# Kernel optimization log

Measured on AMD Instinct MI355X. Metric: run time of the kernel, lower is better.

The kernel has to match this reference:

```python
import jax, jax.numpy as jnp
import numpy as np

DIM_IN = 768
DIM_OUT = 64
SEQ = 4096
BATCH = 4

def setup_inputs() -> dict:
    key = jax.random.key(0)
    ks = jax.random.split(key, 7)
    s = 1.0 / np.sqrt(DIM_IN)
    return {
        "x": jax.random.normal(ks[0], (BATCH, SEQ, DIM_IN), dtype=jnp.float32),
        "wq": jax.random.uniform(ks[1], (DIM_IN, DIM_OUT), jnp.float32, -s, s),
        "bq": jax.random.uniform(ks[2], (DIM_OUT,), jnp.float32, -s, s),
        "wk": jax.random.uniform(ks[3], (DIM_IN, DIM_OUT), jnp.float32, -s, s),
        "bk": jax.random.uniform(ks[4], (DIM_OUT,), jnp.float32, -s, s),
        "wv": jax.random.uniform(ks[5], (DIM_IN, DIM_OUT), jnp.float32, -s, s),
        "bv": jax.random.uniform(ks[6], (DIM_OUT,), jnp.float32, -s, s),
    }

def reference(x, wq, bq, wk, bk, wv, bv):
    # QKV projections: (B, S, D_in) @ (D_in, D_out) + bias
    q = x @ wq + bq
    k = x @ wk + bk
    v = x @ wv + bv
    # full causal attention, scores scaled by sqrt(d_out) AFTER masking (as in source)
    scores = jnp.einsum('bqd,bkd->bqk', q, k)  # (B, S, S)
    seq = x.shape[1]
    causal = jnp.tril(jnp.ones((seq, seq), dtype=bool))  # True = keep
    scores = jnp.where(causal, scores, -jnp.inf)
    scale = 1.0 / np.sqrt(k.shape[-1]).astype(np.float32)
    weights = jax.nn.softmax(scores * scale, axis=-1)
    # dropout_rate = 0.0 -> identity
    return jnp.einsum('bqk,bkd->bqd', weights, v)
```

## Files before the change

### kernel.cpp

```cpp
#include <hip/hip_runtime.h>
#include <hip/hip_bf16.h>

#define BATCH 4
#define SEQ   4096
#define DIN   768
#define DOUT  64

typedef __attribute__((ext_vector_type(4))) float f32x4;
typedef __attribute__((ext_vector_type(8))) short short8;
typedef __attribute__((ext_vector_type(4))) short short4v;

#define QSCALE 0.18033688011112043f

static __device__ __forceinline__ unsigned short f2bf(float f) {
    union { float f; unsigned u; } un; un.f = f;
    unsigned r = un.u + 0x7FFF + ((un.u >> 16) & 1);
    return (unsigned short)(r >> 16);
}
static __device__ __forceinline__ float bf2f(unsigned short h) {
    union { unsigned u; float f; } un; un.u = ((unsigned)h) << 16;
    return un.f;
}

__global__ void wprep_kernel(const float* __restrict__ wq,
                             const float* __restrict__ wk,
                             const float* __restrict__ wv,
                             unsigned short* __restrict__ wF) {
    __shared__ float lds[64][65];
    int o = blockIdx.x / 12, kt = blockIdx.x % 12;
    const float* w = (o == 0) ? wq : (o == 1) ? wk : wv;
    int tid = threadIdx.x;
    int k0 = kt * 64;
    #pragma unroll
    for (int i = 0; i < 16; ++i) {
        int flat = tid + i * 256;
        int kl = flat >> 6, n = flat & 63;
        lds[kl][n] = w[(k0 + kl) * 64 + n];
    }
    __syncthreads();
    int lane = tid & 63;
    int m = lane & 15, g = lane >> 4;
    #pragma unroll
    for (int i = 0; i < 2; ++i) {
        int f = i * 4 + (tid >> 6);
        int t = f >> 1, kcl = f & 1;
        int kc = kt * 2 + kcl;
        int nc = o * 4 + t;
        short8 v;
        #pragma unroll
        for (int j = 0; j < 8; ++j)
            v[j] = (short)f2bf(lds[kcl * 32 + g * 8 + j][t * 16 + m]);
        *(short8*)&wF[(size_t)(nc * 24 + kc) * 512 + lane * 8] = v;
    }
}

__global__ void __launch_bounds__(256) proj_kernel(
        const float* __restrict__ x,
        const float* __restrict__ bq,
        const float* __restrict__ bk,
        const float* __restrict__ bv,
        const unsigned short* __restrict__ wF,
        unsigned short* __restrict__ Qf,
        unsigned short* __restrict__ Kf,
        unsigned short* __restrict__ Vf) {
    __shared__ __align__(16) unsigned short xs[16][776];
    __shared__ unsigned short tr[4][16][24];

    int tid = threadIdx.x;
    int w = tid >> 6;
    int lane = tid & 63;
    int m = lane & 15, g = lane >> 4;
    int r0 = blockIdx.x * 16;

    {
        const float* xbase = x + (size_t)r0 * DIN;
        #pragma unroll
        for (int i = 0; i < 12; ++i) {
            int flat4 = tid + i * 256;
            int row = flat4 / 192;
            int c4 = flat4 - row * 192;
            float4 v = *(const float4*)(xbase + (size_t)row * DIN + c4 * 4);
            short4v sv;
            sv[0] = (short)f2bf(v.x); sv[1] = (short)f2bf(v.y);
            sv[2] = (short)f2bf(v.z); sv[3] = (short)f2bf(v.w);
            *(short4v*)&xs[row][c4 * 4] = sv;
        }
    }
    __syncthreads();

    f32x4 acc[3];
    #pragma unroll
    for (int t = 0; t < 3; ++t) acc[t] = (f32x4){0.f, 0.f, 0.f, 0.f};

    for (int kc = 0; kc < 24; ++kc) {
        short8 af = *(const short8*)&xs[m][kc * 32 + g * 8];
        #pragma unroll
        for (int tt = 0; tt < 3; ++tt) {
            int nc = w * 3 + tt;
            short8 bfrg = *(const short8*)(wF + (size_t)(nc * 24 + kc) * 512 + lane * 8);
            acc[tt] = __builtin_amdgcn_mfma_f32_16x16x32_bf16(af, bfrg, acc[tt], 0, 0, 0);
        }
    }

    int b2 = r0 >> 12;
    int ss = r0 & 4095;
    int s = ss >> 5, half = (ss >> 4) & 1;
    #pragma unroll
    for (int tt = 0; tt < 3; ++tt) {
        int nc = w * 3 + tt;
        int o = nc >> 2;
        int t = nc & 3;
        const float* bias_p = (o == 0) ? bq : (o == 1) ? bk : bv;
        float bias = bias_p[t * 16 + m];
        #pragma unroll
        for (int r = 0; r < 4; ++r) {
            float val = acc[tt][r] + bias;
            if (o == 0) val *= QSCALE;
            tr[w][g * 4 + r][m] = f2bf(val);
        }
        if (o < 2) {
            if (g < 2) {
                short8 v8;
                #pragma unroll
                for (int j = 0; j < 8; ++j) v8[j] = (short)tr[w][m][g * 8 + j];
                unsigned short* dst = (o == 0) ? Qf : Kf;
                int c = t >> 1;
                *(short8*)&dst[(size_t)(blockIdx.x * 2 + c) * 512
                               + (((t & 1) * 2 + g) * 16 + m) * 8] = v8;
            }
        } else {
            if (g < 2) {
                short8 v8;
                #pragma unroll
                for (int j = 0; j < 8; ++j) v8[j] = (short)tr[w][g * 8 + j][m];
                *(short8*)&Vf[((size_t)(b2 * 128 + s) * 4 + t) * 512
                              + ((half * 2 + g) * 16 + m) * 8] = v8;
            }
        }
    }
}

__global__ void __launch_bounds__(512, 4) attn_kernel(
        const unsigned short* __restrict__ Qf,
        const unsigned short* __restrict__ Kf,
        const unsigned short* __restrict__ Vf,
        float* __restrict__ out) {
    __shared__ __align__(16) unsigned short P_lds[8][32][36];
    __shared__ __align__(16) unsigned short pacc[8][16][68];
    __shared__ float pm[8][16];
    __shared__ float pl[8][16];

    int j = blockIdx.x;
    int b = (j & 7) >> 1;
    int pair = 127 - ((j >> 3) * 2 + (j & 1));
    int q0 = pair * 32;
    int nsteps = pair + 1;
    int tid = threadIdx.x;
    int w = tid >> 6;
    int lane = tid & 63;
    int m = lane & 15, g = lane >> 4;

    const unsigned short* Qbase = Qf + (size_t)(b * 256 + pair * 2) * 1024 + lane * 8;
    short8 qf[2][2];
    qf[0][0] = *(const short8*)(Qbase);
    qf[0][1] = *(const short8*)(Qbase + 512);
    qf[1][0] = *(const short8*)(Qbase + 1024);
    qf[1][1] = *(const short8*)(Qbase + 1536);

    short8 onesB = (short8){0,0,0,0,0,0,0,0};
    if (m == 0) {
        #pragma unroll
        for (int jj = 0; jj < 8; ++jj) onesB[jj] = (short)0x3F80;
    }

    f32x4 acc[2][5];
    #pragma unroll
    for (int rt = 0; rt < 2; ++rt)
        #pragma unroll
        for (int t = 0; t < 5; ++t) acc[rt][t] = (f32x4){0.f, 0.f, 0.f, 0.f};
    float mrun[2][4];
    #pragma unroll
    for (int rt = 0; rt < 2; ++rt)
        #pragma unroll
        for (int r = 0; r < 4; ++r) mrun[rt][r] = -INFINITY;

    const unsigned short* Kbase = Kf + (size_t)(b * 256) * 1024 + lane * 8;
    const unsigned short* Vbase = Vf + (size_t)(b * 128) * 2048 + lane * 8;

    for (int s = w; s < nsteps; s += 8) {
        int kv0 = s * 32;
        short8 kf[4];
        kf[0] = *(const short8*)(Kbase + (size_t)s * 2048);
        kf[1] = *(const short8*)(Kbase + (size_t)s * 2048 + 512);
        kf[2] = *(const short8*)(Kbase + (size_t)s * 2048 + 1024);
        kf[3] = *(const short8*)(Kbase + (size_t)s * 2048 + 1536);
        short8 vcur[4];
        #pragma unroll
        for (int t = 0; t < 4; ++t)
            vcur[t] = *(const short8*)(Vbase + (size_t)s * 2048 + t * 512);
        bool last = (s == nsteps - 1);

        #pragma unroll
        for (int rt = 0; rt < 2; ++rt) {
            f32x4 sc[2];
            sc[0] = (f32x4){0.f, 0.f, 0.f, 0.f};
            sc[1] = (f32x4){0.f, 0.f, 0.f, 0.f};
            sc[0] = __builtin_amdgcn_mfma_f32_16x16x32_bf16(qf[rt][0], kf[0], sc[0], 0, 0, 0);
            sc[0] = __builtin_amdgcn_mfma_f32_16x16x32_bf16(qf[rt][1], kf[1], sc[0], 0, 0, 0);
            sc[1] = __builtin_amdgcn_mfma_f32_16x16x32_bf16(qf[rt][0], kf[2], sc[1], 0, 0, 0);
            sc[1] = __builtin_amdgcn_mfma_f32_16x16x32_bf16(qf[rt][1], kf[3], sc[1], 0, 0, 0);

            if (last) {
                #pragma unroll
                for (int tt = 0; tt < 2; ++tt)
                    #pragma unroll
                    for (int r = 0; r < 4; ++r)
                        if (kv0 + tt * 16 + m > q0 + rt * 16 + g * 4 + r) sc[tt][r] = -INFINITY;
            }

            bool need = false;
            #pragma unroll
            for (int r = 0; r < 4; ++r) {
                float th = mrun[rt][r] + 8.0f;
                need = need | (sc[0][r] > th) | (sc[1][r] > th);
            }
            if (__any(need)) {
                float rmax[4];
                #pragma unroll
                for (int r = 0; r < 4; ++r) rmax[r] = fmaxf(sc[0][r], sc[1][r]);
                #pragma unroll
                for (int msk = 1; msk <= 8; msk <<= 1)
                    #pragma unroll
                    for (int r = 0; r < 4; ++r)
                        rmax[r] = fmaxf(rmax[r], __shfl_xor(rmax[r], msk));
                #pragma unroll
                for (int r = 0; r < 4; ++r) {
                    float mnew = fmaxf(mrun[rt][r], rmax[r]);
                    float alpha = __builtin_amdgcn_exp2f(mrun[rt][r] - mnew);
                    mrun[rt][r] = mnew;
                    #pragma unroll
                    for (int t = 0; t < 5; ++t) acc[rt][t][r] *= alpha;
                }
            }

            #pragma unroll
            for (int tt = 0; tt < 2; ++tt)
                #pragma unroll
                for (int r = 0; r < 4; ++r)
                    P_lds[w][rt * 16 + g * 4 + r][tt * 16 + m] =
                        f2bf(__builtin_amdgcn_exp2f(sc[tt][r] - mrun[rt][r]));
            short8 pa = *(const short8*)&P_lds[w][rt * 16 + m][g * 8];

            #pragma unroll
            for (int t = 0; t < 4; ++t)
                acc[rt][t] = __builtin_amdgcn_mfma_f32_16x16x32_bf16(pa, vcur[t], acc[rt][t], 0, 0, 0);
            acc[rt][4] = __builtin_amdgcn_mfma_f32_16x16x32_bf16(pa, onesB, acc[rt][4], 0, 0, 0);
        }
    }

    #pragma unroll
    for (int rt = 0; rt < 2; ++rt) {
        if (m == 0) {
            #pragma unroll
            for (int r = 0; r < 4; ++r) {
                pm[w][g * 4 + r] = mrun[rt][r];
                pl[w][g * 4 + r] = acc[rt][4][r];
            }
        }
        #pragma unroll
        for (int t = 0; t < 4; ++t)
            #pragma unroll
            for (int r = 0; r < 4; ++r)
                pacc[w][g * 4 + r][t * 16 + m] = f2bf(acc[rt][t][r]);
        __syncthreads();

        if (tid < 256) {
            int row = tid >> 4;
            int c4 = (tid & 15) * 4;
            float mmax = pm[0][row];
            #pragma unroll
            for (int w2 = 1; w2 < 8; ++w2) mmax = fmaxf(mmax, pm[w2][row]);
            float lt = 0.f;
            float o0 = 0.f, o1 = 0.f, o2 = 0.f, o3 = 0.f;
            #pragma unroll
            for (int w2 = 0; w2 < 8; ++w2) {
                float sc2 = __builtin_amdgcn_exp2f(pm[w2][row] - mmax);
                lt += pl[w2][row] * sc2;
                short4v pa4 = *(const short4v*)&pacc[w2][row][c4];
                o0 += bf2f((unsigned short)pa4[0]) * sc2;
                o1 += bf2f((unsigned short)pa4[1]) * sc2;
                o2 += bf2f((unsigned short)pa4[2]) * sc2;
                o3 += bf2f((unsigned short)pa4[3]) * sc2;
            }
            float invl = 1.0f / lt;
            float4 res = make_float4(o0 * invl, o1 * invl, o2 * invl, o3 * invl);
            *(float4*)&out[(size_t)(b * SEQ + q0 + rt * 16 + row) * DOUT + c4] = res;
        }
        __syncthreads();
    }
}

extern "C" void kernel_launch(void* const* d_in, const int* in_sizes, int n_in,
                              void* d_out, int out_size, void* d_ws, size_t ws_size,
                              hipStream_t stream) {
    const float* x  = (const float*)d_in[0];
    const float* wq = (const float*)d_in[1];
    const float* bq = (const float*)d_in[2];
    const float* wk = (const float*)d_in[3];
    const float* bk = (const float*)d_in[4];
    const float* wv = (const float*)d_in[5];
    const float* bv = (const float*)d_in[6];
    float* out = (float*)d_out;

    char* ws = (char*)d_ws;
    unsigned short* wF = (unsigned short*)ws;
    unsigned short* Qf = (unsigned short*)(ws + 294912);
    unsigned short* Kf = (unsigned short*)(ws + 294912 + 2097152);
    unsigned short* Vf = (unsigned short*)(ws + 294912 + 4194304);

    wprep_kernel<<<36, 256, 0, stream>>>(wq, wk, wv, wF);
    proj_kernel<<<1024, 256, 0, stream>>>(x, bq, bk, bv, wF, Qf, Kf, Vf);
    attn_kernel<<<512, 512, 0, stream>>>(Qf, Kf, Vf, out);
}
```

Measured before the change: 53.99 us.

## Prefetch next K/V tile in registers and interleave row-tile MFMAs

Software-pipelines the attention loop by loading the K and V fragments for the next step into registers while the current step computes, hiding global load latency. It also restructures the inner loop so both row tiles' QK MFMAs are issued first, then softmax for both, then the PV MFMAs interleaved across row tiles, which raises independent MFMA work available to the scheduler. The cost is higher register pressure from double-buffered K/V fragments and extra score registers, which could lower occupancy.

Result: slower. 109.6 us (+102.9%).

```diff
diff --git a/kernel.cpp b/kernel.cpp
--- a/kernel.cpp
+++ b/kernel.cpp
@@ -187,47 +187,61 @@
     const unsigned short* Kbase = Kf + (size_t)(b * 256) * 1024 + lane * 8;
     const unsigned short* Vbase = Vf + (size_t)(b * 128) * 2048 + lane * 8;
 
+    short8 kf[4], vf[4];
+    if (w < nsteps) {
+        #pragma unroll
+        for (int t = 0; t < 4; ++t) {
+            kf[t] = *(const short8*)(Kbase + (size_t)w * 2048 + t * 512);
+            vf[t] = *(const short8*)(Vbase + (size_t)w * 2048 + t * 512);
+        }
+    }
+
     for (int s = w; s < nsteps; s += 8) {
         int kv0 = s * 32;
-        short8 kf[4];
-        kf[0] = *(const short8*)(Kbase + (size_t)s * 2048);
-        kf[1] = *(const short8*)(Kbase + (size_t)s * 2048 + 512);
-        kf[2] = *(const short8*)(Kbase + (size_t)s * 2048 + 1024);
-        kf[3] = *(const short8*)(Kbase + (size_t)s * 2048 + 1536);
-        short8 vcur[4];
-        #pragma unroll
-        for (int t = 0; t < 4; ++t)
-            vcur[t] = *(const short8*)(Vbase + (size_t)s * 2048 + t * 512);
         bool last = (s == nsteps - 1);
-
+        int sn = s + 8;
+        short8 kn[4], vn[4];
+        if (sn < nsteps) {
+            #pragma unroll
+            for (int t = 0; t < 4; ++t) {
+                kn[t] = *(const short8*)(Kbase + (size_t)sn * 2048 + t * 512);
+                vn[t] = *(const short8*)(Vbase + (size_t)sn * 2048 + t * 512);
+            }
+        }
+
+        f32x4 sc[2][2];
         #pragma unroll
         for (int rt = 0; rt < 2; ++rt) {
-            f32x4 sc[2];
-            sc[0] = (f32x4){0.f, 0.f, 0.f, 0.f};
-            sc[1] = (f32x4){0.f, 0.f, 0.f, 0.f};
-            sc[0] = __builtin_amdgcn_mfma_f32_16x16x32_bf16(qf[rt][0], kf[0], sc[0], 0, 0, 0);
-            sc[0] = __builtin_amdgcn_mfma_f32_16x16x32_bf16(qf[rt][1], kf[1], sc[0], 0, 0, 0);
-            sc[1] = __builtin_amdgcn_mfma_f32_16x16x32_bf16(qf[rt][0], kf[2], sc[1], 0, 0, 0);
-            sc[1] = __builtin_amdgcn_mfma_f32_16x16x32_bf16(qf[rt][1], kf[3], sc[1], 0, 0, 0);
-
-            if (last) {
+            sc[rt][0] = (f32x4){0.f, 0.f, 0.f, 0.f};
+            sc[rt][1] = (f32x4){0.f, 0.f, 0.f, 0.f};
+            sc[rt][0] = __builtin_amdgcn_mfma_f32_16x16x32_bf16(qf[rt][0], kf[0], sc[rt][0], 0, 0, 0);
+            sc[rt][0] = __builtin_amdgcn_mfma_f32_16x16x32_bf16(qf[rt][1], kf[1], sc[rt][0], 0, 0, 0);
+            sc[rt][1] = __builtin_amdgcn_mfma_f32_16x16x32_bf16(qf[rt][0], kf[2], sc[rt][1], 0, 0, 0);
+            sc[rt][1] = __builtin_amdgcn_mfma_f32_16x16x32_bf16(qf[rt][1], kf[3], sc[rt][1], 0, 0, 0);
+        }
+        if (last) {
+            #pragma unroll
+            for (int rt = 0; rt < 2; ++rt)
                 #pragma unroll
                 for (int tt = 0; tt < 2; ++tt)
                     #pragma unroll
                     for (int r = 0; r < 4; ++r)
-                        if (kv0 + tt * 16 + m > q0 + rt * 16 + g * 4 + r) sc[tt][r] = -INFINITY;
-            }
-
+                        if (kv0 + tt * 16 + m > q0 + rt * 16 + g * 4 + r)
+                            sc[rt][tt][r] = -INFINITY;
+        }
+
+        #pragma unroll
+        for (int rt = 0; rt < 2; ++rt) {
             bool need = false;
             #pragma unroll
             for (int r = 0; r < 4; ++r) {
                 float th = mrun[rt][r] + 8.0f;
-                need = need | (sc[0][r] > th) | (sc[1][r] > th);
+                need = need | (sc[rt][0][r] > th) | (sc[rt][1][r] > th);
             }
             if (__any(need)) {
                 float rmax[4];
                 #pragma unroll
-                for (int r = 0; r < 4; ++r) rmax[r] = fmaxf(sc[0][r], sc[1][r]);
+                for (int r = 0; r < 4; ++r) rmax[r] = fmaxf(sc[rt][0][r], sc[rt][1][r]);
                 #pragma unroll
                 for (int msk = 1; msk <= 8; msk <<= 1)
                     #pragma unroll
@@ -242,19 +256,27 @@
                     for (int t = 0; t < 5; ++t) acc[rt][t][r] *= alpha;
                 }
             }
-
             #pragma unroll
             for (int tt = 0; tt < 2; ++tt)
                 #pragma unroll
                 for (int r = 0; r < 4; ++r)
                     P_lds[w][rt * 16 + g * 4 + r][tt * 16 + m] =
-                        f2bf(__builtin_amdgcn_exp2f(sc[tt][r] - mrun[rt][r]));
-            short8 pa = *(const short8*)&P_lds[w][rt * 16 + m][g * 8];
-
-            #pragma unroll
-            for (int t = 0; t < 4; ++t)
-                acc[rt][t] = __builtin_amdgcn_mfma_f32_16x16x32_bf16(pa, vcur[t], acc[rt][t], 0, 0, 0);
-            acc[rt][4] = __builtin_amdgcn_mfma_f32_16x16x32_bf16(pa, onesB, acc[rt][4], 0, 0, 0);
+                        f2bf(__builtin_amdgcn_exp2f(sc[rt][tt][r] - mrun[rt][r]));
+        }
+
+        short8 pa0 = *(const short8*)&P_lds[w][m][g * 8];
+        short8 pa1 = *(const short8*)&P_lds[w][16 + m][g * 8];
+        #pragma unroll
+        for (int t = 0; t < 4; ++t) {
+            acc[0][t] = __builtin_amdgcn_mfma_f32_16x16x32_bf16(pa0, vf[t], acc[0][t], 0, 0, 0);
+            acc[1][t] = __builtin_amdgcn_mfma_f32_16x16x32_bf16(pa1, vf[t], acc[1][t], 0, 0, 0);
+        }
+        acc[0][4] = __builtin_amdgcn_mfma_f32_16x16x32_bf16(pa0, onesB, acc[0][4], 0, 0, 0);
+        acc[1][4] = __builtin_amdgcn_mfma_f32_16x16x32_bf16(pa1, onesB, acc[1][4], 0, 0, 0);
+
+        if (sn < nsteps) {
+            #pragma unroll
+            for (int t = 0; t < 4; ++t) { kf[t] = kn[t]; vf[t] = vn[t]; }
         }
     }
 
```
